# Performance work log

Hardware: AMD Instinct MI355X
Metric: run time of the kernel (lower is better)

Reference implementation:

```python
import jax, jax.numpy as jnp
import numpy as np

# Dimensions (production-scale molecular density evaluation)
S = 5        # n_species (element types)
NR = 3       # n_radial functions per element (max_funs)
NA = 3       # max_angular_moment -> l in {1,2,3}
F = NR * NA  # total terms (k=1)
B, M, N = 8, 4096, 64  # batch molecules, grid points, atoms
EPS = 1e-12


def setup_inputs() -> dict:
    key = jax.random.key(0)
    k1, k2, k3, k4, k5, k6 = jax.random.split(key, 6)
    dv = jax.random.normal(k1, (B, M, N, 3), jnp.float32)           # displacement grid_point - atom
    coefficients = jax.random.normal(k2, (B, N, F, 3), jnp.float32)  # per-atom anisotropic coeff vectors
    labels = jax.random.randint(k3, (B, N), 0, S)                    # species index per atom
    a = jax.random.uniform(k4, (S, NR), jnp.float32, 0.5, 2.0)       # amplitudes
    b = jax.random.uniform(k5, (S, NR), jnp.float32, 0.5, 3.0)       # exponents
    p = jax.random.uniform(k6, (S, NR), jnp.float32, 0.0, 2.0)       # radial powers
    return {"dv": dv, "coefficients": coefficients, "labels": labels, "a": a, "b": b, "p": p}


def _legendre(x, l):
    # Legendre polynomial P_l(x) for l in {1,2,3}; l broadcasts over the term dim
    p1 = x
    p2 = 0.5 * (3.0 * x * x - 1.0)
    p3 = 0.5 * (5.0 * x * x * x - 3.0 * x)
    return jnp.where(l == 1, p1, jnp.where(l == 2, p2, p3))


def reference(dv, coefficients, labels, a, b, p):
    # expand radial params across the angular terms (repeat_interleave along dim 1): [S, F]
    a_e = jnp.repeat(a, NA, axis=1)
    b_e = jnp.repeat(b, NA, axis=1)
    p_e = jnp.repeat(p, NA, axis=1)
    # per-atom label gather (expand_parameter): [B, N, F]
    a_g = a_e[labels]
    b_g = b_e[labels]
    p_g = p_e[labels]
    # distances: [B, M, N]
    r = jnp.linalg.norm(dv, axis=-1)
    r4 = r[..., None]                                   # [B, M, N, 1]
    # generalized exponential kernel a * r^p * exp(-b r): [B, M, N, F]
    kern = a_g[:, None] * r4 ** p_g[:, None] * jnp.exp(-b_g[:, None] * r4)
    # anisotropic angular part: |c| * P_l(cos angle(dv, c))
    cnorm = jnp.linalg.norm(coefficients, axis=-1)      # [B, N, F]
    cunit = coefficients / jnp.maximum(cnorm[..., None], EPS)
    cos = jnp.einsum('bmnd,bnfd->bmnf', dv, cunit) / jnp.maximum(r4, EPS)
    l_arr = (jnp.arange(F) % NA) + 1                    # 1,2,3 cycling (qi pattern)
    q = _legendre(cos, l_arr)                           # [B, M, N, F]
    dens = kern * cnorm[:, None] * q                    # [B, M, N, F]
    # accumulate over terms, then over atoms (density += k; density.sum(2))
    return dens.sum(axis=(2, 3))                        # [B, M]
```

## Files before the change

kernel.cpp:

```cpp
#include <hip/hip_runtime.h>

#define Bb  8
#define Mm  4096
#define Nn  64
#define Ff  9
#define Ss  5
#define NRr 3

constexpr int REC = 16;

__global__ void HarmonicGen_precompute(
    const float* __restrict__ coef,
    const int*   __restrict__ labels,
    const float* __restrict__ pa,
    const float* __restrict__ pb,
    const float* __restrict__ pp,
    float*       __restrict__ table)
{
    const int i = blockIdx.x * 256 + threadIdx.x;
    if (i >= Bb * Nn * NRr) return;
    const int j  = i % NRr;
    const int bn = i / NRr;
    const int s  = labels[bn];
    const float av = pa[s * NRr + j];
    const float bv = pb[s * NRr + j];
    const float pv = pp[s * NRr + j];
    float* rec = table + (size_t)i * REC;
    rec[0] = bv * 1.44269504088896340736f;
    rec[1] = pv;
    rec[2] = 0.0f; rec[3] = 0.0f;
#pragma unroll
    for (int lm = 0; lm < 3; ++lm) {
        const int f = j * 3 + lm;
        const float* c = coef + ((size_t)bn * Ff + f) * 3;
        const float cx = c[0], cy = c[1], cz = c[2];
        const float cn  = sqrtf(cx * cx + cy * cy + cz * cz);
        const float inv = 1.0f / fmaxf(cn, 1e-12f);
        rec[4 + lm * 4 + 0] = av * cn;
        rec[4 + lm * 4 + 1] = cx * inv;
        rec[4 + lm * 4 + 2] = cy * inv;
        rec[4 + lm * 4 + 3] = cz * inv;
    }
}

constexpr int MT  = 64;
constexpr int PAD = 193;

__global__ __launch_bounds__(256, 2)
void HarmonicGenAMD_25786983645325_kernel(
    const float* __restrict__ dv,
    const float* __restrict__ table,
    float*       __restrict__ out)
{
    __shared__ __align__(16) float dvs[MT * PAD];
    __shared__ float red[4 * MT];

    const int tid = threadIdx.x;
    const int blk = blockIdx.x;
    const int b   = blk >> 6;
    const int m0  = (blk & 63) * MT;

    const float* g = dv + ((size_t)b * Mm + m0) * (Nn * 3);
    for (int i = tid * 4; i < MT * Nn * 3; i += 256 * 4) {
        const int row = i / 192;
        const int col = i - row * 192;
        const float4 v = *(const float4*)(g + (size_t)row * 192 + col);
        float* d = &dvs[row * PAD + col];
        d[0] = v.x; d[1] = v.y; d[2] = v.z; d[3] = v.w;
    }
    __syncthreads();

    const int lane = tid & 63;
    const int wid  = tid >> 6;
    const float* drow = &dvs[lane * PAD];
    const float4* tb = (const float4*)(table + (size_t)b * Nn * NRr * REC);

    float acc = 0.0f;
#pragma unroll 4
    for (int t = 0; t < 16; ++t) {
        const int n = wid * 16 + t;
        const float x = drow[n * 3 + 0];
        const float y = drow[n * 3 + 1];
        const float z = drow[n * 3 + 2];
        const float r2   = x * x + y * y + z * z;
        const float r    = __builtin_amdgcn_sqrtf(r2);
        const float rinv = __builtin_amdgcn_rcpf(fmaxf(r, 1e-12f));
        const float l2r  = 0.5f * __builtin_amdgcn_logf(r2);

        const float4* rec = tb + (size_t)n * (NRr * 4);
#pragma unroll
        for (int j = 0; j < NRr; ++j) {
            const float4 h = rec[j * 4 + 0];
            const float ek = __builtin_amdgcn_exp2f(__fmaf_rn(h.y, l2r, -h.x * r));
#pragma unroll
            for (int lm = 0; lm < 3; ++lm) {
                const float4 e = rec[j * 4 + 1 + lm];
                const float kern = e.x * ek;
                const float cosv = (x * e.y + y * e.z + z * e.w) * rinv;
                float q;
                if (lm == 0)      q = cosv;
                else if (lm == 1) q = __fmaf_rn(1.5f * cosv, cosv, -0.5f);
                else              q = cosv * __fmaf_rn(2.5f * cosv, cosv, -1.5f);
                acc = __fmaf_rn(kern, q, acc);
            }
        }
    }

    red[wid * MT + lane] = acc;
    __syncthreads();
    if (tid < MT) {
        const float s = red[tid] + red[MT + tid] + red[2 * MT + tid] + red[3 * MT + tid];
        out[(size_t)b * Mm + m0 + tid] = s;
    }
}

extern "C" void kernel_launch(void* const* d_in, const int* in_sizes, int n_in,
                              void* d_out, int out_size, void* d_ws, size_t ws_size,
                              hipStream_t stream) {
    const float* dv   = (const float*)d_in[0];
    const float* coef = (const float*)d_in[1];
    const int*   lab  = (const int*)d_in[2];
    const float* pa   = (const float*)d_in[3];
    const float* pb   = (const float*)d_in[4];
    const float* pp   = (const float*)d_in[5];
    float* out   = (float*)d_out;
    float* table = (float*)d_ws;

    HarmonicGen_precompute<<<(Bb * Nn * NRr + 255) / 256, 256, 0, stream>>>(
        coef, lab, pa, pb, pp, table);

    dim3 grid(Bb * (Mm / MT));
    HarmonicGenAMD_25786983645325_kernel<<<grid, 256, 0, stream>>>(dv, table, out);
}
```

Measured before the change: 95.67 us.

## Repack per-atom parameter table and hoist direction normalization out of term loop

Reorganizes the precomputed table into one 48-float record per atom (radial exponents and powers packed first, then nine coefficient records), and marks the atom base index as wave-uniform via readfirstlane so table reads can become scalar loads. The main kernel uses rsq instead of sqrt plus rcp, normalizes the displacement once per atom instead of scaling each cosine, and drops the occupancy hint from the launch bounds. The aim is fewer vector loads and ALU ops per atom, at the cost of a less constrained register budget and a slightly different rsq-based numerics path for r near zero.

```diff
diff --git a/kernel.cpp b/kernel.cpp
--- a/kernel.cpp
+++ b/kernel.cpp
@@ -7,7 +7,7 @@
 #define Ss  5
 #define NRr 3
 
-constexpr int REC = 16;
+constexpr int REC = 48;
 
 __global__ void HarmonicGen_precompute(
     const float* __restrict__ coef,
@@ -18,42 +18,40 @@
     float*       __restrict__ table)
 {
     const int i = blockIdx.x * 256 + threadIdx.x;
-    if (i >= Bb * Nn * NRr) return;
-    const int j  = i % NRr;
-    const int bn = i / NRr;
-    const int s  = labels[bn];
-    const float av = pa[s * NRr + j];
-    const float bv = pb[s * NRr + j];
-    const float pv = pp[s * NRr + j];
+    if (i >= Bb * Nn) return;
+    const int s = labels[i];
     float* rec = table + (size_t)i * REC;
-    rec[0] = bv * 1.44269504088896340736f;
-    rec[1] = pv;
-    rec[2] = 0.0f; rec[3] = 0.0f;
 #pragma unroll
-    for (int lm = 0; lm < 3; ++lm) {
-        const int f = j * 3 + lm;
-        const float* c = coef + ((size_t)bn * Ff + f) * 3;
+    for (int j = 0; j < NRr; ++j) {
+        rec[j * 2 + 0] = pb[s * NRr + j] * 1.44269504088896340736f;
+        rec[j * 2 + 1] = pp[s * NRr + j];
+    }
+    rec[6] = 0.0f; rec[7] = 0.0f;
+#pragma unroll
+    for (int f = 0; f < Ff; ++f) {
+        const int j = f / 3;
+        const float* c = coef + ((size_t)i * Ff + f) * 3;
         const float cx = c[0], cy = c[1], cz = c[2];
         const float cn  = sqrtf(cx * cx + cy * cy + cz * cz);
         const float inv = 1.0f / fmaxf(cn, 1e-12f);
-        rec[4 + lm * 4 + 0] = av * cn;
-        rec[4 + lm * 4 + 1] = cx * inv;
-        rec[4 + lm * 4 + 2] = cy * inv;
-        rec[4 + lm * 4 + 3] = cz * inv;
+        rec[8 + f * 4 + 0] = pa[s * NRr + j] * cn;
+        rec[8 + f * 4 + 1] = cx * inv;
+        rec[8 + f * 4 + 2] = cy * inv;
+        rec[8 + f * 4 + 3] = cz * inv;
     }
 }
 
 constexpr int MT  = 64;
 constexpr int PAD = 193;
 
-__global__ __launch_bounds__(256, 2)
+__global__ __launch_bounds__(256)
 void HarmonicGenAMD_25786983645325_kernel(
     const float* __restrict__ dv,
     const float* __restrict__ table,
     float*       __restrict__ out)
 {
     __shared__ __align__(16) float dvs[MT * PAD];
-    __shared__ float red[4 * MT];
+    __shared__ float red[256];
 
     const int tid = threadIdx.x;
     const int blk = blockIdx.x;
@@ -70,47 +68,47 @@
     }
     __syncthreads();
 
-    const int lane = tid & 63;
-    const int wid  = tid >> 6;
-    const float* drow = &dvs[lane * PAD];
-    const float4* tb = (const float4*)(table + (size_t)b * Nn * NRr * REC);
+    const int lane  = tid & 63;
+    const int nbase = __builtin_amdgcn_readfirstlane((tid >> 6) * 16);
+    const float* tb   = table + ((size_t)b * Nn + nbase) * REC;
+    const float* drow = &dvs[lane * PAD + nbase * 3];
 
     float acc = 0.0f;
 #pragma unroll 4
     for (int t = 0; t < 16; ++t) {
-        const int n = wid * 16 + t;
-        const float x = drow[n * 3 + 0];
-        const float y = drow[n * 3 + 1];
-        const float z = drow[n * 3 + 2];
-        const float r2   = x * x + y * y + z * z;
-        const float r    = __builtin_amdgcn_sqrtf(r2);
-        const float rinv = __builtin_amdgcn_rcpf(fmaxf(r, 1e-12f));
+        const float* rec = tb + t * REC;
+        const float x = drow[t * 3 + 0];
+        const float y = drow[t * 3 + 1];
+        const float z = drow[t * 3 + 2];
+        const float r2   = __fmaf_rn(x, x, __fmaf_rn(y, y, z * z));
+        const float rinv = __builtin_amdgcn_rsqf(r2);
+        const float r    = r2 * rinv;
         const float l2r  = 0.5f * __builtin_amdgcn_logf(r2);
+        const float dnx = x * rinv, dny = y * rinv, dnz = z * rinv;
 
-        const float4* rec = tb + (size_t)n * (NRr * 4);
+        const float4 h0 = *(const float4*)(rec);
+        const float2 h1 = *(const float2*)(rec + 4);
+        float ek[3];
+        ek[0] = __builtin_amdgcn_exp2f(__fmaf_rn(h0.y, l2r, -h0.x * r));
+        ek[1] = __builtin_amdgcn_exp2f(__fmaf_rn(h0.w, l2r, -h0.z * r));
+        ek[2] = __builtin_amdgcn_exp2f(__fmaf_rn(h1.y, l2r, -h1.x * r));
 #pragma unroll
-        for (int j = 0; j < NRr; ++j) {
-            const float4 h = rec[j * 4 + 0];
-            const float ek = __builtin_amdgcn_exp2f(__fmaf_rn(h.y, l2r, -h.x * r));
-#pragma unroll
-            for (int lm = 0; lm < 3; ++lm) {
-                const float4 e = rec[j * 4 + 1 + lm];
-                const float kern = e.x * ek;
-                const float cosv = (x * e.y + y * e.z + z * e.w) * rinv;
-                float q;
-                if (lm == 0)      q = cosv;
-                else if (lm == 1) q = __fmaf_rn(1.5f * cosv, cosv, -0.5f);
-                else              q = cosv * __fmaf_rn(2.5f * cosv, cosv, -1.5f);
-                acc = __fmaf_rn(kern, q, acc);
-            }
+        for (int f = 0; f < Ff; ++f) {
+            const float4 e = *(const float4*)(rec + 8 + f * 4);
+            const float c = __fmaf_rn(dnx, e.y, __fmaf_rn(dny, e.z, dnz * e.w));
+            float q;
+            if      (f % 3 == 0) q = c;
+            else if (f % 3 == 1) q = __fmaf_rn(1.5f * c, c, -0.5f);
+            else                 q = c * __fmaf_rn(2.5f * c, c, -1.5f);
+            acc = __fmaf_rn(e.x * ek[f / 3], q, acc);
         }
     }
 
-    red[wid * MT + lane] = acc;
+    red[tid] = acc;
     __syncthreads();
     if (tid < MT) {
-        const float s = red[tid] + red[MT + tid] + red[2 * MT + tid] + red[3 * MT + tid];
-        out[(size_t)b * Mm + m0 + tid] = s;
+        out[(size_t)b * Mm + m0 + tid] =
+            red[tid] + red[MT + tid] + red[2 * MT + tid] + red[3 * MT + tid];
     }
 }
 
@@ -126,8 +124,7 @@
     float* out   = (float*)d_out;
     float* table = (float*)d_ws;
 
-    HarmonicGen_precompute<<<(Bb * Nn * NRr + 255) / 256, 256, 0, stream>>>(
-        coef, lab, pa, pb, pp, table);
+    HarmonicGen_precompute<<<2, 256, 0, stream>>>(coef, lab, pa, pb, pp, table);
 
     dim3 grid(Bb * (Mm / MT));
     HarmonicGenAMD_25786983645325_kernel<<<grid, 256, 0, stream>>>(dv, table, out);
```

Measured after the change: 88.49 us. 7.5% less time.
